# Kernel tuning notes

Hardware: AMD Instinct MI355X
Metric: run time of the kernel (lower is better)

The kernel has to match this reference:

```python
import jax, jax.numpy as jnp
import numpy as np

NUM_CLUSTERS = 64
MARGIN = 1.0
B = 8192


def setup_inputs() -> dict:
    key = jax.random.key(0)
    k1, k2, k3 = jax.random.split(key, 3)
    features = jax.random.normal(k1, (B, 128), dtype=jnp.float32)
    cluster_labels = jax.random.randint(k2, (B,), 0, NUM_CLUSTERS)
    manifold_coords = jax.random.normal(k3, (B, 2), dtype=jnp.float32)
    return {"features": features, "cluster_labels": cluster_labels,
            "manifold_coords": manifold_coords}


def _pairwise_dist(x):
    # Euclidean cdist via the (|a|^2 + |b|^2 - 2ab) identity; [B, B]
    sq = jnp.sum(x * x, axis=1)
    d2 = sq[:, None] + sq[None, :] - 2.0 * (x @ x.T)
    d2 = jnp.maximum(d2, 0.0)
    # Overwrite diagonal (same-point zero distance) to avoid sqrt(0); diagonal
    # entries only feed the discarded intra-cluster M[i,i] values.
    idx = jnp.arange(x.shape[0])
    d2 = jnp.where(idx[:, None] == idx[None, :], 1.0, d2)
    return jnp.sqrt(d2)


def reference(features, cluster_labels, manifold_coords):
    # Equivalent to the torch double loop over unique labels: min pairwise
    # distance between every cluster pair (i < j), hinge with margin, mean.
    d = _pairwise_dist(manifold_coords)                       # [B, B]
    # segment-min over rows then columns -> min distance per cluster pair
    row_min = jax.ops.segment_min(d, cluster_labels, num_segments=NUM_CLUSTERS)      # [K, B]
    M = jax.ops.segment_min(row_min.T, cluster_labels, num_segments=NUM_CLUSTERS).T  # [K, K]
    upper = jnp.triu(jnp.ones((NUM_CLUSTERS, NUM_CLUSTERS), dtype=bool), k=1)
    hinge = jax.nn.relu(MARGIN - M)
    num_pairs = NUM_CLUSTERS * (NUM_CLUSTERS - 1) // 2
    return jnp.sum(jnp.where(upper, hinge, 0.0)) / num_pairs
```

## Files before the change

kernel.cpp:

```cpp
#include <hip/hip_runtime.h>

#define B_N 8192
#define K_CL 64
#define CAP 256
#define NPAIR 2016
#define INF_F 3.0e38f


__global__ __launch_bounds__(256) void gather_kernel(
    const int* __restrict__ labels, const float* __restrict__ coords,
    float2* __restrict__ lists, int* __restrict__ cnts) {
    int c = blockIdx.x;
    int tid = threadIdx.x, lane = tid & 63, wave = tid >> 6;
    __shared__ int wsum[4];

    int4 lb[8];
    float4 cr[16];
    const int4*   l4 = reinterpret_cast<const int4*>(labels);
    const float4* c4 = reinterpret_cast<const float4*>(coords);
#pragma unroll
    for (int k = 0; k < 8; ++k) {
        int v4 = tid + k * 256;
        lb[k]       = l4[v4];
        cr[2*k]     = c4[2*v4];
        cr[2*k + 1] = c4[2*v4 + 1];
    }
    int mcnt = 0;
#pragma unroll
    for (int k = 0; k < 8; ++k)
        mcnt += (lb[k].x==c) + (lb[k].y==c) + (lb[k].z==c) + (lb[k].w==c);

    int incl = mcnt;
#pragma unroll
    for (int d = 1; d < 64; d <<= 1) {
        int u = __shfl_up(incl, d, 64);
        if (lane >= d) incl += u;
    }
    if (lane == 63) wsum[wave] = incl;
    __syncthreads();
    int wbase = 0;
#pragma unroll
    for (int w = 0; w < 4; ++w) wbase += (w < wave) ? wsum[w] : 0;
    int base = wbase + incl - mcnt;
    if (tid == 255) cnts[c] = min(base + mcnt, CAP);

    int pos = base;
#pragma unroll
    for (int k = 0; k < 8; ++k) {
        float2 p0 = make_float2(cr[2*k].x,     cr[2*k].y);
        float2 p1 = make_float2(cr[2*k].z,     cr[2*k].w);
        float2 p2 = make_float2(cr[2*k + 1].x, cr[2*k + 1].y);
        float2 p3 = make_float2(cr[2*k + 1].z, cr[2*k + 1].w);
        if (lb[k].x == c) { if (pos < CAP) lists[c*CAP + pos] = p0; pos++; }
        if (lb[k].y == c) { if (pos < CAP) lists[c*CAP + pos] = p1; pos++; }
        if (lb[k].z == c) { if (pos < CAP) lists[c*CAP + pos] = p2; pos++; }
        if (lb[k].w == c) { if (pos < CAP) lists[c*CAP + pos] = p3; pos++; }
    }
}

__global__ __launch_bounds__(256) void pair_min_kernel(
    const float2* __restrict__ lists, const int* __restrict__ cnts,
    float* __restrict__ hinges) {
    int ci = blockIdx.x, cj = blockIdx.y;
    if (ci >= cj) return;
    int nI = min(cnts[ci], CAP), nJ = min(cnts[cj], CAP);
    int tid = threadIdx.x;
    __shared__ float2 ipt[CAP], jpt[CAP];
    if (tid < nJ) jpt[tid] = lists[cj * CAP + tid];
    if (tid < nI) ipt[tid] = lists[ci * CAP + tid];
    __syncthreads();

    int half = (nJ + 1) >> 1;
    int j0 = (tid & 1) ? half : 0;
    int j1 = (tid & 1) ? nJ : half;
    float m0 = INF_F, m1 = INF_F, m2 = INF_F, m3 = INF_F;
    for (int i = tid >> 1; i < nI; i += 128) {
        float2 pi = ipt[i];
        int j = j0;
        for (; j + 3 < j1; j += 4) {
            float2 a = jpt[j], b = jpt[j+1], c = jpt[j+2], d = jpt[j+3];
            float dx0 = pi.x - a.x, dy0 = pi.y - a.y;
            float dx1 = pi.x - b.x, dy1 = pi.y - b.y;
            float dx2 = pi.x - c.x, dy2 = pi.y - c.y;
            float dx3 = pi.x - d.x, dy3 = pi.y - d.y;
            m0 = fminf(m0, dx0*dx0 + dy0*dy0);
            m1 = fminf(m1, dx1*dx1 + dy1*dy1);
            m2 = fminf(m2, dx2*dx2 + dy2*dy2);
            m3 = fminf(m3, dx3*dx3 + dy3*dy3);
        }
        for (; j < j1; ++j) {
            float dx = pi.x - jpt[j].x, dy = pi.y - jpt[j].y;
            m0 = fminf(m0, dx*dx + dy*dy);
        }
    }
    float myMin = fminf(fminf(m0, m1), fminf(m2, m3));

    for (int off = 32; off > 0; off >>= 1)
        myMin = fminf(myMin, __shfl_down(myMin, off, 64));
    __shared__ float wmin[4];
    int wave = tid >> 6, lane = tid & 63;
    if (lane == 0) wmin[wave] = myMin;
    __syncthreads();
    if (tid == 0) {
        float m = fminf(fminf(wmin[0], wmin[1]), fminf(wmin[2], wmin[3]));
        float h = 1.0f - sqrtf(m);
        hinges[ci * K_CL + cj] = h > 0.0f ? h : 0.0f;
    }
}

__global__ void reduce_hinge_kernel(const float* __restrict__ hinges,
                                    float* __restrict__ out) {
    int tid = threadIdx.x;
    float s = 0.0f;
    for (int p = tid; p < K_CL * K_CL; p += 256) {
        int ci = p >> 6, cj = p & 63;
        if (ci < cj) s += hinges[p];
    }
    for (int off = 32; off > 0; off >>= 1)
        s += __shfl_down(s, off, 64);
    __shared__ float wsum[4];
    int wave = tid >> 6, lane = tid & 63;
    if (lane == 0) wsum[wave] = s;
    __syncthreads();
    if (tid == 0)
        out[0] = (wsum[0] + wsum[1] + wsum[2] + wsum[3]) / (float)NPAIR;
}

extern "C" void kernel_launch(void* const* d_in, const int* in_sizes, int n_in,
                              void* d_out, int out_size, void* d_ws, size_t ws_size,
                              hipStream_t stream) {
    const int*   labels = (const int*)d_in[1];
    const float* coords = (const float*)d_in[2];
    float* out = (float*)d_out;

    float2* lists  = (float2*)d_ws;
    int*    cnts   = (int*)((char*)d_ws + 2 * K_CL * CAP * sizeof(float));
    float*  hinges = (float*)((char*)cnts + 256);

    gather_kernel<<<K_CL, 256, 0, stream>>>(labels, coords, lists, cnts);
    dim3 grid(K_CL, K_CL);
    pair_min_kernel<<<grid, 256, 0, stream>>>(lists, cnts, hinges);
    reduce_hinge_kernel<<<1, 256, 0, stream>>>(hinges, out);
}
```

Before: 29.50 us.

## Split gather into per-segment blocks and concatenate segments in pair kernel

The gather kernel now launches 64x8 blocks, one per cluster and input segment, each scanning 1024 points instead of 8192. Per-segment counts are prefix-summed inside the pair-min kernel, which concatenates the segment lists into shared memory. This spreads gather work over more blocks to cut serial per-block latency, at the cost of extra count loads and strided copies in the pair kernel. A per-segment cap of 48 points per cluster could truncate inputs if a segment holds more.

```diff
diff --git a/kernel.cpp b/kernel.cpp
--- a/kernel.cpp
+++ b/kernel.cpp
@@ -2,7 +2,9 @@
 
 #define B_N 8192
 #define K_CL 64
-#define CAP 256
+#define SEG 8
+#define CAP_SEG 48
+#define LCAP (SEG * CAP_SEG)
 #define NPAIR 2016
 #define INF_F 3.0e38f
 
@@ -10,25 +12,16 @@
 __global__ __launch_bounds__(256) void gather_kernel(
     const int* __restrict__ labels, const float* __restrict__ coords,
     float2* __restrict__ lists, int* __restrict__ cnts) {
-    int c = blockIdx.x;
+    int c = blockIdx.x, q = blockIdx.y;
     int tid = threadIdx.x, lane = tid & 63, wave = tid >> 6;
     __shared__ int wsum[4];
 
-    int4 lb[8];
-    float4 cr[16];
-    const int4*   l4 = reinterpret_cast<const int4*>(labels);
-    const float4* c4 = reinterpret_cast<const float4*>(coords);
-#pragma unroll
-    for (int k = 0; k < 8; ++k) {
-        int v4 = tid + k * 256;
-        lb[k]       = l4[v4];
-        cr[2*k]     = c4[2*v4];
-        cr[2*k + 1] = c4[2*v4 + 1];
-    }
-    int mcnt = 0;
-#pragma unroll
-    for (int k = 0; k < 8; ++k)
-        mcnt += (lb[k].x==c) + (lb[k].y==c) + (lb[k].z==c) + (lb[k].w==c);
+    int v4 = q * 256 + tid;
+    int4   lb = reinterpret_cast<const int4*>(labels)[v4];
+    float4 ca = reinterpret_cast<const float4*>(coords)[2 * v4];
+    float4 cb = reinterpret_cast<const float4*>(coords)[2 * v4 + 1];
+
+    int mcnt = (lb.x == c) + (lb.y == c) + (lb.z == c) + (lb.w == c);
 
     int incl = mcnt;
 #pragma unroll
@@ -42,20 +35,14 @@
 #pragma unroll
     for (int w = 0; w < 4; ++w) wbase += (w < wave) ? wsum[w] : 0;
     int base = wbase + incl - mcnt;
-    if (tid == 255) cnts[c] = min(base + mcnt, CAP);
+    if (tid == 255) cnts[c * SEG + q] = min(base + mcnt, CAP_SEG);
 
+    float2* seg = lists + (c * SEG + q) * CAP_SEG;
     int pos = base;
-#pragma unroll
-    for (int k = 0; k < 8; ++k) {
-        float2 p0 = make_float2(cr[2*k].x,     cr[2*k].y);
-        float2 p1 = make_float2(cr[2*k].z,     cr[2*k].w);
-        float2 p2 = make_float2(cr[2*k + 1].x, cr[2*k + 1].y);
-        float2 p3 = make_float2(cr[2*k + 1].z, cr[2*k + 1].w);
-        if (lb[k].x == c) { if (pos < CAP) lists[c*CAP + pos] = p0; pos++; }
-        if (lb[k].y == c) { if (pos < CAP) lists[c*CAP + pos] = p1; pos++; }
-        if (lb[k].z == c) { if (pos < CAP) lists[c*CAP + pos] = p2; pos++; }
-        if (lb[k].w == c) { if (pos < CAP) lists[c*CAP + pos] = p3; pos++; }
-    }
+    if (lb.x == c) { if (pos < CAP_SEG) seg[pos] = make_float2(ca.x, ca.y); pos++; }
+    if (lb.y == c) { if (pos < CAP_SEG) seg[pos] = make_float2(ca.z, ca.w); pos++; }
+    if (lb.z == c) { if (pos < CAP_SEG) seg[pos] = make_float2(cb.x, cb.y); pos++; }
+    if (lb.w == c) { if (pos < CAP_SEG) seg[pos] = make_float2(cb.z, cb.w); pos++; }
 }
 
 __global__ __launch_bounds__(256) void pair_min_kernel(
@@ -63,11 +50,25 @@
     float* __restrict__ hinges) {
     int ci = blockIdx.x, cj = blockIdx.y;
     if (ci >= cj) return;
-    int nI = min(cnts[ci], CAP), nJ = min(cnts[cj], CAP);
     int tid = threadIdx.x;
-    __shared__ float2 ipt[CAP], jpt[CAP];
-    if (tid < nJ) jpt[tid] = lists[cj * CAP + tid];
-    if (tid < nI) ipt[tid] = lists[ci * CAP + tid];
+
+    int cI[SEG + 1], cJ[SEG + 1];
+    cI[0] = 0; cJ[0] = 0;
+#pragma unroll
+    for (int s = 0; s < SEG; ++s) {
+        cI[s + 1] = cI[s] + cnts[ci * SEG + s];
+        cJ[s + 1] = cJ[s] + cnts[cj * SEG + s];
+    }
+    int nI = cI[SEG], nJ = cJ[SEG];
+
+    __shared__ float2 ipt[LCAP], jpt[LCAP];
+#pragma unroll
+    for (int s = 0; s < SEG; ++s) {
+        int nqi = cI[s + 1] - cI[s];
+        if (tid < nqi) ipt[cI[s] + tid] = lists[(ci * SEG + s) * CAP_SEG + tid];
+        int nqj = cJ[s + 1] - cJ[s];
+        if (tid < nqj) jpt[cJ[s] + tid] = lists[(cj * SEG + s) * CAP_SEG + tid];
+    }
     __syncthreads();
 
     int half = (nJ + 1) >> 1;
@@ -134,11 +135,12 @@
     float* out = (float*)d_out;
 
     float2* lists  = (float2*)d_ws;
-    int*    cnts   = (int*)((char*)d_ws + 2 * K_CL * CAP * sizeof(float));
-    float*  hinges = (float*)((char*)cnts + 256);
+    int*    cnts   = (int*)((char*)d_ws + (size_t)K_CL * SEG * CAP_SEG * sizeof(float2));
+    float*  hinges = (float*)((char*)cnts + K_CL * SEG * sizeof(int));
 
-    gather_kernel<<<K_CL, 256, 0, stream>>>(labels, coords, lists, cnts);
-    dim3 grid(K_CL, K_CL);
-    pair_min_kernel<<<grid, 256, 0, stream>>>(lists, cnts, hinges);
+    dim3 ggrid(K_CL, SEG);
+    gather_kernel<<<ggrid, 256, 0, stream>>>(labels, coords, lists, cnts);
+    dim3 pgrid(K_CL, K_CL);
+    pair_min_kernel<<<pgrid, 256, 0, stream>>>(lists, cnts, hinges);
     reduce_hinge_kernel<<<1, 256, 0, stream>>>(hinges, out);
 }
```

After: 33.90 us. 14.9% more time.

## Fuse cluster gather into pair kernel and launch only upper-triangle pairs

Applied to the files above, without the earlier changes.

Removes the separate gather kernel. Each of the 2016 pair blocks now rescans all 8192 labels, counts both clusters with a packed prefix scan, and compacts the matching coordinates straight into shared memory. This drops one kernel launch, the global round trip for the lists, and the 4096-block grid in which half the blocks exit at once. In exchange every block reads the full 32 KB label array, which should mostly hit cache, and the 16-bit packing in the scan assumes per-wave counts stay below 65536.

```diff
diff --git a/kernel.cpp b/kernel.cpp
--- a/kernel.cpp
+++ b/kernel.cpp
@@ -7,30 +7,33 @@
 #define INF_F 3.0e38f
 
 
-__global__ __launch_bounds__(256) void gather_kernel(
-    const int* __restrict__ labels, const float* __restrict__ coords,
-    float2* __restrict__ lists, int* __restrict__ cnts) {
-    int c = blockIdx.x;
+__global__ __launch_bounds__(256) void pair_kernel(
+    const int* __restrict__ labels, const float2* __restrict__ coords,
+    float* __restrict__ hinges) {
+    int p = blockIdx.x;
+    int ci = 0, rem = p;
+    while (rem >= K_CL - 1 - ci) { rem -= K_CL - 1 - ci; ci++; }
+    int cj = ci + 1 + rem;
     int tid = threadIdx.x, lane = tid & 63, wave = tid >> 6;
+
+    __shared__ float2 ipt[CAP], jpt[CAP];
     __shared__ int wsum[4];
+    __shared__ float wred[4];
 
     int4 lb[8];
-    float4 cr[16];
-    const int4*   l4 = reinterpret_cast<const int4*>(labels);
-    const float4* c4 = reinterpret_cast<const float4*>(coords);
+#pragma unroll
+    for (int k = 0; k < 8; ++k)
+        lb[k] = reinterpret_cast<const int4*>(labels)[tid + k * 256];
+
+    int cntI = 0, cntJ = 0;
 #pragma unroll
     for (int k = 0; k < 8; ++k) {
-        int v4 = tid + k * 256;
-        lb[k]       = l4[v4];
-        cr[2*k]     = c4[2*v4];
-        cr[2*k + 1] = c4[2*v4 + 1];
+        cntI += (lb[k].x==ci) + (lb[k].y==ci) + (lb[k].z==ci) + (lb[k].w==ci);
+        cntJ += (lb[k].x==cj) + (lb[k].y==cj) + (lb[k].z==cj) + (lb[k].w==cj);
     }
-    int mcnt = 0;
-#pragma unroll
-    for (int k = 0; k < 8; ++k)
-        mcnt += (lb[k].x==c) + (lb[k].y==c) + (lb[k].z==c) + (lb[k].w==c);
 
-    int incl = mcnt;
+    int pack = (cntI << 16) | cntJ;
+    int incl = pack;
 #pragma unroll
     for (int d = 1; d < 64; d <<= 1) {
         int u = __shfl_up(incl, d, 64);
@@ -38,36 +41,31 @@
     }
     if (lane == 63) wsum[wave] = incl;
     __syncthreads();
-    int wbase = 0;
+    int wbase = 0, tot = 0;
 #pragma unroll
-    for (int w = 0; w < 4; ++w) wbase += (w < wave) ? wsum[w] : 0;
-    int base = wbase + incl - mcnt;
-    if (tid == 255) cnts[c] = min(base + mcnt, CAP);
+    for (int w = 0; w < 4; ++w) {
+        wbase += (w < wave) ? wsum[w] : 0;
+        tot += wsum[w];
+    }
+    int basep = wbase + incl - pack;
+    int posI = basep >> 16, posJ = basep & 0xffff;
+    int nI = min(tot >> 16, CAP), nJ = min(tot & 0xffff, CAP);
 
-    int pos = base;
 #pragma unroll
     for (int k = 0; k < 8; ++k) {
-        float2 p0 = make_float2(cr[2*k].x,     cr[2*k].y);
-        float2 p1 = make_float2(cr[2*k].z,     cr[2*k].w);
-        float2 p2 = make_float2(cr[2*k + 1].x, cr[2*k + 1].y);
-        float2 p3 = make_float2(cr[2*k + 1].z, cr[2*k + 1].w);
-        if (lb[k].x == c) { if (pos < CAP) lists[c*CAP + pos] = p0; pos++; }
-        if (lb[k].y == c) { if (pos < CAP) lists[c*CAP + pos] = p1; pos++; }
-        if (lb[k].z == c) { if (pos < CAP) lists[c*CAP + pos] = p2; pos++; }
-        if (lb[k].w == c) { if (pos < CAP) lists[c*CAP + pos] = p3; pos++; }
+        int v4 = tid + k * 256;
+        int lab[4] = {lb[k].x, lb[k].y, lb[k].z, lb[k].w};
+#pragma unroll
+        for (int cc = 0; cc < 4; ++cc) {
+            if (lab[cc] == ci) {
+                if (posI < CAP) ipt[posI] = coords[4 * v4 + cc];
+                posI++;
+            } else if (lab[cc] == cj) {
+                if (posJ < CAP) jpt[posJ] = coords[4 * v4 + cc];
+                posJ++;
+            }
+        }
     }
-}
-
-__global__ __launch_bounds__(256) void pair_min_kernel(
-    const float2* __restrict__ lists, const int* __restrict__ cnts,
-    float* __restrict__ hinges) {
-    int ci = blockIdx.x, cj = blockIdx.y;
-    if (ci >= cj) return;
-    int nI = min(cnts[ci], CAP), nJ = min(cnts[cj], CAP);
-    int tid = threadIdx.x;
-    __shared__ float2 ipt[CAP], jpt[CAP];
-    if (tid < nJ) jpt[tid] = lists[cj * CAP + tid];
-    if (tid < nI) ipt[tid] = lists[ci * CAP + tid];
     __syncthreads();
 
     int half = (nJ + 1) >> 1;
@@ -97,14 +95,12 @@
 
     for (int off = 32; off > 0; off >>= 1)
         myMin = fminf(myMin, __shfl_down(myMin, off, 64));
-    __shared__ float wmin[4];
-    int wave = tid >> 6, lane = tid & 63;
-    if (lane == 0) wmin[wave] = myMin;
+    if (lane == 0) wred[wave] = myMin;
     __syncthreads();
     if (tid == 0) {
-        float m = fminf(fminf(wmin[0], wmin[1]), fminf(wmin[2], wmin[3]));
+        float m = fminf(fminf(wred[0], wred[1]), fminf(wred[2], wred[3]));
         float h = 1.0f - sqrtf(m);
-        hinges[ci * K_CL + cj] = h > 0.0f ? h : 0.0f;
+        hinges[p] = h > 0.0f ? h : 0.0f;
     }
 }
 
@@ -112,10 +108,7 @@
                                     float* __restrict__ out) {
     int tid = threadIdx.x;
     float s = 0.0f;
-    for (int p = tid; p < K_CL * K_CL; p += 256) {
-        int ci = p >> 6, cj = p & 63;
-        if (ci < cj) s += hinges[p];
-    }
+    for (int p = tid; p < NPAIR; p += 256) s += hinges[p];
     for (int off = 32; off > 0; off >>= 1)
         s += __shfl_down(s, off, 64);
     __shared__ float wsum[4];
@@ -129,16 +122,11 @@
 extern "C" void kernel_launch(void* const* d_in, const int* in_sizes, int n_in,
                               void* d_out, int out_size, void* d_ws, size_t ws_size,
                               hipStream_t stream) {
-    const int*   labels = (const int*)d_in[1];
-    const float* coords = (const float*)d_in[2];
-    float* out = (float*)d_out;
+    const int*    labels = (const int*)d_in[1];
+    const float2* coords = (const float2*)d_in[2];
+    float* out    = (float*)d_out;
+    float* hinges = (float*)d_ws;
 
-    float2* lists  = (float2*)d_ws;
-    int*    cnts   = (int*)((char*)d_ws + 2 * K_CL * CAP * sizeof(float));
-    float*  hinges = (float*)((char*)cnts + 256);
-
-    gather_kernel<<<K_CL, 256, 0, stream>>>(labels, coords, lists, cnts);
-    dim3 grid(K_CL, K_CL);
-    pair_min_kernel<<<grid, 256, 0, stream>>>(lists, cnts, hinges);
+    pair_kernel<<<NPAIR, 256, 0, stream>>>(labels, coords, hinges);
     reduce_hinge_kernel<<<1, 256, 0, stream>>>(hinges, out);
 }
```

After: 36.42 us. +23.5%, slower.
